# Kernel optimization log

Measured on AMD Instinct MI355X. Metric: run time of the kernel, lower is better.

Reference implementation:

```python
import jax, jax.numpy as jnp
import numpy as np

DIM = 64
HEADS = 4            # self.num_heads = 2 * num_heads(=2)
SMK = 5
KS = 7
EPS = 1e-5
SCALE = (DIM // HEADS) ** -0.5


def pool_mat(n, out=7):
    # AdaptiveAvgPool2d bin matrix: P[i, j] = 1/size if floor(i*n/out) <= j < ceil((i+1)*n/out)
    P = np.zeros((out, n), np.float32)
    for i in range(out):
        s = (i * n) // out
        e = -((-(i + 1) * n) // out)
        P[i, s:e] = 1.0 / (e - s)
    return jnp.asarray(P)


def bn(x, g, b, m, v):
    # inference BatchNorm2d on [B,C,H,W]
    return (x - m[:, None, None]) * (g[:, None, None] * jax.lax.rsqrt(v[:, None, None] + EPS)) + b[:, None, None]


def conv1x1(x, w):
    return jnp.einsum('oi,bihw->bohw', w, x)


def rpb_bias(rpb, H, W, k):
    # replicate apply_rpb gather indexing (incl. the flip over flattened HW)
    rs = 2 * k - 1
    ih0 = np.arange(k)
    idx_k = (ih0[:, None] * rs + ih0[None, :]).reshape(-1)        # [k*k]
    rh = np.ones(k, np.int64); rh[k // 2] = H - (k - 1)
    rw = np.ones(k, np.int64); rw[k // 2] = W - (k - 1)
    ih = np.repeat(ih0, rh)                                       # [H]
    iw = np.repeat(ih0, rw)                                       # [W]
    bias_hw = ih[:, None] * rs + iw[None, :]                      # [H,W]
    bias_idx = (bias_hw[..., None] + idx_k).reshape(-1, k * k)[::-1].copy()  # [H*W,k*k]
    flat = rpb.reshape(rpb.shape[0], -1)                          # [G, rs*rs]
    return flat[:, bias_idx].reshape(1, rpb.shape[0], H, W, k * k)


def na2d_av(attn, value, k):
    # NATTEN-style neighborhood AV: window start clamped to stay in-bounds
    B, G, H, W, _ = attn.shape
    si = np.clip(np.arange(H) - k // 2, 0, H - k)
    sj = np.clip(np.arange(W) - k // 2, 0, W - k)
    ii = si[:, None] + np.arange(k)    # [H,k]
    jj = sj[:, None] + np.arange(k)    # [W,k]
    v = value[:, :, ii][:, :, :, :, jj]         # [B,G,H,k,W,k,C]
    a = attn.reshape(B, G, H, W, k, k)
    return jnp.einsum('bghwij,bghiwjc->bghwc', a, v)


def reference(x, wq_w, wq_g, wq_b, wq_m, wq_v,
              wk_w, wk_g, wk_b, wk_m, wk_v,
              proj_w, proj_b, rpb1, rpb2,
              dy_w, dy_g, dy_b, dy_m, dy_v):
    B, C, H, W = x.shape
    G = HEADS
    q, kctx = jnp.split(x, 2, axis=1)                      # [B,C/2,H,W] each
    q = bn(conv1x1(q, wq_w), wq_g, wq_b, wq_m, wq_v) * SCALE
    Ph, Pw = pool_mat(H), pool_mat(W)
    kp = jnp.einsum('ph,bchw,qw->bcpq', Ph, kctx, Pw)      # adaptive avg pool to 7x7
    k = bn(conv1x1(kp, wk_w), wk_g, wk_b, wk_m, wk_v)
    q = q.reshape(B, G, -1, H * W)                          # b g c n
    k = k.reshape(B, G, -1, 49)                             # b g c l
    w = jnp.einsum('bgcn,bgcl->bgnl', q, k)
    w = w.transpose(0, 3, 1, 2)                             # b l g n
    w = jnp.einsum('ol,blgn->bogn', proj_w, w) + proj_b[None, :, None, None]  # b (74) g n
    w = w.transpose(0, 2, 3, 1).reshape(B, G, H, W, SMK * SMK + KS * KS)
    attn1 = w[..., :SMK * SMK]
    attn2 = w[..., SMK * SMK:]
    attn1 = jax.nn.softmax(attn1 + rpb_bias(rpb1, H, W, SMK), axis=-1)
    attn2 = jax.nn.softmax(attn2 + rpb_bias(rpb2, H, W, KS), axis=-1)
    c = C // (2 * G)
    value = x.reshape(B, 2, G, c, H, W).transpose(1, 0, 2, 4, 5, 3)  # m b g h w c
    x1 = na2d_av(attn1, value[0], SMK)
    x2 = na2d_av(attn2, value[1], KS)
    out = jnp.concatenate([x1, x2], axis=1)                 # b (2g) h w c
    out = out.transpose(0, 1, 4, 2, 3).reshape(B, C, H, W)  # b (g c) h w
    return bn(conv1x1(out, dy_w), dy_g, dy_b, dy_m, dy_v)


def setup_inputs() -> dict:
    key = jax.random.key(0)
    ks = jax.random.split(key, 20)
    h = DIM // 2
    def bnp(k):
        k1, k2, k3, k4 = jax.random.split(k, 4)
        return (jax.random.uniform(k1, (0,)),)  # unused
    inp = {
        'x': jax.random.normal(ks[0], (8, DIM, 64, 64), jnp.float32),
        'wq_w': jax.random.normal(ks[1], (h, h), jnp.float32) * (h ** -0.5),
        'wq_g': jax.random.uniform(ks[2], (h,), jnp.float32, 0.5, 1.5),
        'wq_b': jax.random.normal(ks[3], (h,), jnp.float32) * 0.1,
        'wq_m': jax.random.normal(ks[4], (h,), jnp.float32) * 0.1,
        'wq_v': jax.random.uniform(ks[5], (h,), jnp.float32, 0.5, 1.5),
        'wk_w': jax.random.normal(ks[6], (h, h), jnp.float32) * (h ** -0.5),
        'wk_g': jax.random.uniform(ks[7], (h,), jnp.float32, 0.5, 1.5),
        'wk_b': jax.random.normal(ks[8], (h,), jnp.float32) * 0.1,
        'wk_m': jax.random.normal(ks[9], (h,), jnp.float32) * 0.1,
        'wk_v': jax.random.uniform(ks[10], (h,), jnp.float32, 0.5, 1.5),
        'proj_w': jax.random.normal(ks[11], (SMK * SMK + KS * KS, 49), jnp.float32) * (49 ** -0.5),
        'proj_b': jax.random.normal(ks[12], (SMK * SMK + KS * KS,), jnp.float32) * 0.02,
        'rpb1': jax.random.normal(ks[13], (HEADS, 2 * SMK - 1, 2 * SMK - 1), jnp.float32) * 0.02,
        'rpb2': jax.random.normal(ks[14], (HEADS, 2 * KS - 1, 2 * KS - 1), jnp.float32) * 0.02,
        'dy_w': jax.random.normal(ks[15], (DIM, DIM), jnp.float32) * (DIM ** -0.5),
        'dy_g': jax.random.uniform(ks[16], (DIM,), jnp.float32, 0.5, 1.5),
        'dy_b': jax.random.normal(ks[17], (DIM,), jnp.float32) * 0.1,
        'dy_m': jax.random.normal(ks[18], (DIM,), jnp.float32) * 0.1,
        'dy_v': jax.random.uniform(ks[19], (DIM,), jnp.float32, 0.5, 1.5),
    }
    return inp
```

## Files before the change

### kernel.cpp

```cpp
#include <hip/hip_runtime.h>

#define EPSV 1e-5f

__global__ __launch_bounds__(256) void pool_k_kernel(
    const float* __restrict__ x,
    const float* __restrict__ wk_w, const float* __restrict__ wk_g,
    const float* __restrict__ wk_b, const float* __restrict__ wk_m,
    const float* __restrict__ wk_v, float* __restrict__ kbuf)
{
  const int b = blockIdx.x / 7;
  const int p = blockIdx.x % 7;
  const int tid = threadIdx.x;
  __shared__ float s_tmp[32 * 64];
  __shared__ float s_kp[32 * 7];

  const int sh = (p * 64) / 7, eh = ((p + 1) * 64 + 6) / 7;
  const float invH = 1.0f / (float)(eh - sh);
  for (int idx = tid; idx < 2048; idx += 256) {
    const int c = idx >> 6, ww = idx & 63;
    const float* xp = x + ((size_t)(b * 64 + 32 + c)) * 4096 + ww;
    float s = 0.f;
    for (int hh = sh; hh < eh; ++hh) s += xp[hh * 64];
    s_tmp[idx] = s * invH;
  }
  __syncthreads();
  if (tid < 224) {
    const int c = tid / 7, q = tid % 7;
    const int sw = (q * 64) / 7, ew = ((q + 1) * 64 + 6) / 7;
    float s = 0.f;
    for (int ww = sw; ww < ew; ++ww) s += s_tmp[c * 64 + ww];
    s_kp[c * 7 + q] = s / (float)(ew - sw);
  }
  __syncthreads();
  if (tid < 224) {
    const int o = tid / 7, q = tid % 7;
    float s = 0.f;
#pragma unroll
    for (int i = 0; i < 32; i++) s += wk_w[o * 32 + i] * s_kp[i * 7 + q];
    const float sc = wk_g[o] * rsqrtf(wk_v[o] + EPSV);
    kbuf[(size_t)b * 1568 + o * 49 + p * 7 + q] = (s - wk_m[o]) * sc + wk_b[o];
  }
}

__global__ __launch_bounds__(512, 4) void contmix_main(
    const float* __restrict__ x,
    const float* __restrict__ wq_w, const float* __restrict__ wq_g,
    const float* __restrict__ wq_b, const float* __restrict__ wq_m,
    const float* __restrict__ wq_v,
    const float* __restrict__ proj_w, const float* __restrict__ proj_b,
    const float* __restrict__ rpb1, const float* __restrict__ rpb2,
    const float* __restrict__ dy_w, const float* __restrict__ dy_g,
    const float* __restrict__ dy_b, const float* __restrict__ dy_m,
    const float* __restrict__ dy_v,
    const float* __restrict__ kbuf,
    float* __restrict__ out)
{
  __shared__ float s_rpb1[4 * 81];
  __shared__ float s_rpb2[4 * 169];
  __shared__ float s_val[64 * 64];

  const int bx = blockIdx.x;
  const int b = bx >> 6;
  const int h = bx & 63;
  const int tid = threadIdx.x;
  const int w = tid & 63;
  const int bru = __builtin_amdgcn_readfirstlane(tid >> 8);
  const int gu  = __builtin_amdgcn_readfirstlane((tid >> 6) & 3);

  for (int i = tid; i < 324; i += 512) s_rpb1[i] = rpb1[i];
  for (int i = tid; i < 676; i += 512) s_rpb2[i] = rpb2[i];
  __syncthreads();

  const float* xb = x + (size_t)b * 64 * 4096;

  float q8[8];
#pragma unroll
  for (int o = 0; o < 8; o++) q8[o] = 0.f;
  {
    const float* wqr = wq_w + gu * 8 * 32;
#pragma unroll
    for (int i = 0; i < 32; i++) {
      const float xv = xb[i * 4096 + h * 64 + w];
#pragma unroll
      for (int o = 0; o < 8; o++) q8[o] += wqr[o * 32 + i] * xv;
    }
#pragma unroll
    for (int o = 0; o < 8; o++) {
      const int oc = gu * 8 + o;
      const float s = wq_g[oc] * rsqrtf(wq_v[oc] + EPSV);
      q8[o] = (q8[o] * s + (wq_b[oc] - wq_m[oc] * s)) * 0.25f;
    }
  }

  float wv[49];
  {
    const float* kkb = kbuf + (size_t)b * 1568 + gu * 392;
#pragma unroll
    for (int l = 0; l < 49; l++) {
      float s = 0.f;
#pragma unroll
      for (int c = 0; c < 8; c++) s += q8[c] * kkb[c * 49 + l];
      wv[l] = s;
    }
  }

  const int ph = 63 - h, pw = 63 - w;

  if (bru == 0) {
    const int bih5 = ph - min(max(ph - 2, 0), 59);
    const int biw5 = pw - min(max(pw - 2, 0), 59);
    const int si5 = min(max(h - 2, 0), 59), sj5 = min(max(w - 2, 0), 59);
    float l1[25];
#pragma unroll
    for (int o = 0; o < 25; o++) {
      float s = proj_b[o];
#pragma unroll
      for (int l = 0; l < 49; l++) s += proj_w[o * 49 + l] * wv[l];
      l1[o] = s;
    }
    const float* rp1 = s_rpb1 + gu * 81 + bih5 * 9 + biw5;
#pragma unroll
    for (int ki = 0; ki < 5; ki++)
#pragma unroll
      for (int kj = 0; kj < 5; kj++) l1[ki * 5 + kj] += rp1[ki * 9 + kj];

    float mx = l1[0];
#pragma unroll
    for (int o = 1; o < 25; o++) mx = fmaxf(mx, l1[o]);
    float sum = 0.f;
#pragma unroll
    for (int o = 0; o < 25; o++) {
      const float e = __expf(l1[o] - mx);
      l1[o] = e;
      sum += e;
    }
    const float inv = 1.f / sum;

    float acc[8];
#pragma unroll
    for (int c = 0; c < 8; c++) acc[c] = 0.f;
    const float* vb = xb + gu * 8 * 4096;
#pragma unroll
    for (int i = 0; i < 5; i++) {
      const float* vr = vb + (si5 + i) * 64 + sj5;
#pragma unroll
      for (int j = 0; j < 5; j++) {
        const float a = l1[i * 5 + j];
#pragma unroll
        for (int c = 0; c < 8; c++) acc[c] += a * vr[c * 4096 + j];
      }
    }
#pragma unroll
    for (int c = 0; c < 8; c++) s_val[(gu * 8 + c) * 64 + w] = acc[c] * inv;
  } else {
    const int bih7 = ph - min(max(ph - 3, 0), 57);
    const int biw7 = pw - min(max(pw - 3, 0), 57);
    const int si7 = min(max(h - 3, 0), 57), sj7 = min(max(w - 3, 0), 57);
    float l2[49];
#pragma unroll
    for (int o = 0; o < 49; o++) {
      float s = proj_b[25 + o];
#pragma unroll
      for (int l = 0; l < 49; l++) s += proj_w[(25 + o) * 49 + l] * wv[l];
      l2[o] = s;
    }
    const float* rp2 = s_rpb2 + gu * 169 + bih7 * 13 + biw7;
#pragma unroll
    for (int ki = 0; ki < 7; ki++)
#pragma unroll
      for (int kj = 0; kj < 7; kj++) l2[ki * 7 + kj] += rp2[ki * 13 + kj];

    float mx = l2[0];
#pragma unroll
    for (int o = 1; o < 49; o++) mx = fmaxf(mx, l2[o]);
    float sum = 0.f;
#pragma unroll
    for (int o = 0; o < 49; o++) {
      const float e = __expf(l2[o] - mx);
      l2[o] = e;
      sum += e;
    }
    const float inv = 1.f / sum;

    float acc[8];
#pragma unroll
    for (int c = 0; c < 8; c++) acc[c] = 0.f;
    const float* vb = xb + (32 + gu * 8) * 4096;
#pragma unroll
    for (int i = 0; i < 7; i++) {
      const float* vr = vb + (si7 + i) * 64 + sj7;
#pragma unroll
      for (int j = 0; j < 7; j++) {
        const float a = l2[i * 7 + j];
#pragma unroll
        for (int c = 0; c < 8; c++) acc[c] += a * vr[c * 4096 + j];
      }
    }
#pragma unroll
    for (int c = 0; c < 8; c++) s_val[(32 + gu * 8 + c) * 64 + w] = acc[c] * inv;
  }

  __syncthreads();

  {
    const int ogu = __builtin_amdgcn_readfirstlane(tid >> 6);
    float facc[8];
#pragma unroll
    for (int oo = 0; oo < 8; oo++) facc[oo] = 0.f;
    const float* dwr = dy_w + ogu * 8 * 64;
#pragma unroll
    for (int i = 0; i < 64; i++) {
      const float v = s_val[i * 64 + w];
#pragma unroll
      for (int oo = 0; oo < 8; oo++) facc[oo] += dwr[oo * 64 + i] * v;
    }
#pragma unroll
    for (int oo = 0; oo < 8; oo++) {
      const int oc = ogu * 8 + oo;
      const float sc = dy_g[oc] * rsqrtf(dy_v[oc] + EPSV);
      out[((size_t)(b * 64 + oc)) * 4096 + h * 64 + w] =
          (facc[oo] - dy_m[oc]) * sc + dy_b[oc];
    }
  }
}

extern "C" void kernel_launch(void* const* d_in, const int* in_sizes, int n_in,
                              void* d_out, int out_size, void* d_ws, size_t ws_size,
                              hipStream_t stream)
{
  const float* x      = (const float*)d_in[0];
  const float* wq_w   = (const float*)d_in[1];
  const float* wq_g   = (const float*)d_in[2];
  const float* wq_b   = (const float*)d_in[3];
  const float* wq_m   = (const float*)d_in[4];
  const float* wq_v   = (const float*)d_in[5];
  const float* wk_w   = (const float*)d_in[6];
  const float* wk_g   = (const float*)d_in[7];
  const float* wk_b   = (const float*)d_in[8];
  const float* wk_m   = (const float*)d_in[9];
  const float* wk_v   = (const float*)d_in[10];
  const float* proj_w = (const float*)d_in[11];
  const float* proj_b = (const float*)d_in[12];
  const float* rpb1   = (const float*)d_in[13];
  const float* rpb2   = (const float*)d_in[14];
  const float* dy_w   = (const float*)d_in[15];
  const float* dy_g   = (const float*)d_in[16];
  const float* dy_b   = (const float*)d_in[17];
  const float* dy_m   = (const float*)d_in[18];
  const float* dy_v   = (const float*)d_in[19];

  float* kbuf = (float*)d_ws;

  pool_k_kernel<<<56, 256, 0, stream>>>(x, wk_w, wk_g, wk_b, wk_m, wk_v, kbuf);
  contmix_main<<<512, 512, 0, stream>>>(x, wq_w, wq_g, wq_b, wq_m, wq_v,
                                        proj_w, proj_b, rpb1, rpb2,
                                        dy_w, dy_g, dy_b, dy_m, dy_v,
                                        kbuf, (float*)d_out);
}
```

Baseline: 196.0 us.

## Pre-transpose weights and stream k-projection fused into logit accumulation

Adds a prep kernel that writes transposed, padded copies of wq, proj and dy weights to workspace, and stores the pooled key buffer transposed so each position's 8 channels are contiguous. The main kernel no longer keeps a 49-element wv array; it computes each wv[l] on the fly and scatters it into the logit accumulators, which cuts register pressure and lets weight loads be contiguous and vectorizable. The occupancy hint is relaxed from 4 to 2 blocks per unit. The cost is an extra kernel launch and a changed register/occupancy balance.

```diff
diff --git a/kernel.cpp b/kernel.cpp
--- a/kernel.cpp
+++ b/kernel.cpp
@@ -1,12 +1,44 @@
 #include <hip/hip_runtime.h>
 
 #define EPSV 1e-5f
+
+#define OFF_PW1T 12544
+#define OFF_PW2T 14112
+#define OFF_WQT  17248
+#define OFF_DYT  18272
+
+__global__ __launch_bounds__(512) void prep_weights(
+    const float* __restrict__ wq_w, const float* __restrict__ proj_w,
+    const float* __restrict__ dy_w, float* __restrict__ ws)
+{
+  const int t = blockIdx.x * 512 + threadIdx.x;
+  float* wqT  = ws + OFF_WQT;
+  float* pw1T = ws + OFF_PW1T;
+  float* pw2T = ws + OFF_PW2T;
+  float* dyT  = ws + OFF_DYT;
+  for (int idx = t; idx < 1024; idx += 8192) {
+    const int i = idx >> 5, o = idx & 31;
+    wqT[idx] = wq_w[o * 32 + i];
+  }
+  for (int idx = t; idx < 1568; idx += 8192) {
+    const int l = idx >> 5, o = idx & 31;
+    pw1T[idx] = (o < 25) ? proj_w[o * 49 + l] : 0.f;
+  }
+  for (int idx = t; idx < 3136; idx += 8192) {
+    const int l = idx >> 6, o = idx & 63;
+    pw2T[idx] = (o < 49) ? proj_w[(25 + o) * 49 + l] : 0.f;
+  }
+  for (int idx = t; idx < 4096; idx += 8192) {
+    const int i = idx >> 6, o = idx & 63;
+    dyT[idx] = dy_w[o * 64 + i];
+  }
+}
 
 __global__ __launch_bounds__(256) void pool_k_kernel(
     const float* __restrict__ x,
     const float* __restrict__ wk_w, const float* __restrict__ wk_g,
     const float* __restrict__ wk_b, const float* __restrict__ wk_m,
-    const float* __restrict__ wk_v, float* __restrict__ kbuf)
+    const float* __restrict__ wk_v, float* __restrict__ kbufT)
 {
   const int b = blockIdx.x / 7;
   const int p = blockIdx.x % 7;
@@ -38,21 +70,21 @@
 #pragma unroll
     for (int i = 0; i < 32; i++) s += wk_w[o * 32 + i] * s_kp[i * 7 + q];
     const float sc = wk_g[o] * rsqrtf(wk_v[o] + EPSV);
-    kbuf[(size_t)b * 1568 + o * 49 + p * 7 + q] = (s - wk_m[o]) * sc + wk_b[o];
-  }
-}
-
-__global__ __launch_bounds__(512, 4) void contmix_main(
+    const int g = o >> 3, c = o & 7, l = p * 7 + q;
+    kbufT[(((size_t)b * 4 + g) * 49 + l) * 8 + c] =
+        (s - wk_m[o]) * sc + wk_b[o];
+  }
+}
+
+__global__ __launch_bounds__(512, 2) void contmix_main(
     const float* __restrict__ x,
-    const float* __restrict__ wq_w, const float* __restrict__ wq_g,
-    const float* __restrict__ wq_b, const float* __restrict__ wq_m,
-    const float* __restrict__ wq_v,
-    const float* __restrict__ proj_w, const float* __restrict__ proj_b,
+    const float* __restrict__ wq_g, const float* __restrict__ wq_b,
+    const float* __restrict__ wq_m, const float* __restrict__ wq_v,
+    const float* __restrict__ proj_b,
     const float* __restrict__ rpb1, const float* __restrict__ rpb2,
-    const float* __restrict__ dy_w, const float* __restrict__ dy_g,
-    const float* __restrict__ dy_b, const float* __restrict__ dy_m,
-    const float* __restrict__ dy_v,
-    const float* __restrict__ kbuf,
+    const float* __restrict__ dy_g, const float* __restrict__ dy_b,
+    const float* __restrict__ dy_m, const float* __restrict__ dy_v,
+    const float* __restrict__ ws,
     float* __restrict__ out)
 {
   __shared__ float s_rpb1[4 * 81];
@@ -77,12 +109,12 @@
 #pragma unroll
   for (int o = 0; o < 8; o++) q8[o] = 0.f;
   {
-    const float* wqr = wq_w + gu * 8 * 32;
+    const float* wqt = ws + OFF_WQT + gu * 8;
 #pragma unroll
     for (int i = 0; i < 32; i++) {
       const float xv = xb[i * 4096 + h * 64 + w];
 #pragma unroll
-      for (int o = 0; o < 8; o++) q8[o] += wqr[o * 32 + i] * xv;
+      for (int o = 0; o < 8; o++) q8[o] += wqt[i * 32 + o] * xv;
     }
 #pragma unroll
     for (int o = 0; o < 8; o++) {
@@ -92,17 +124,7 @@
     }
   }
 
-  float wv[49];
-  {
-    const float* kkb = kbuf + (size_t)b * 1568 + gu * 392;
-#pragma unroll
-    for (int l = 0; l < 49; l++) {
-      float s = 0.f;
-#pragma unroll
-      for (int c = 0; c < 8; c++) s += q8[c] * kkb[c * 49 + l];
-      wv[l] = s;
-    }
-  }
+  const float* kt = ws + ((size_t)b * 4 + gu) * 392;
 
   const int ph = 63 - h, pw = 63 - w;
 
@@ -112,11 +134,16 @@
     const int si5 = min(max(h - 2, 0), 59), sj5 = min(max(w - 2, 0), 59);
     float l1[25];
 #pragma unroll
-    for (int o = 0; o < 25; o++) {
-      float s = proj_b[o];
-#pragma unroll
-      for (int l = 0; l < 49; l++) s += proj_w[o * 49 + l] * wv[l];
-      l1[o] = s;
+    for (int o = 0; o < 25; o++) l1[o] = proj_b[o];
+    const float* p1 = ws + OFF_PW1T;
+#pragma unroll 4
+    for (int l = 0; l < 49; l++) {
+      float a = 0.f;
+#pragma unroll
+      for (int c = 0; c < 8; c++) a += q8[c] * kt[l * 8 + c];
+      const float* pr = p1 + l * 32;
+#pragma unroll
+      for (int o = 0; o < 25; o++) l1[o] += pr[o] * a;
     }
     const float* rp1 = s_rpb1 + gu * 81 + bih5 * 9 + biw5;
 #pragma unroll
@@ -158,11 +185,16 @@
     const int si7 = min(max(h - 3, 0), 57), sj7 = min(max(w - 3, 0), 57);
     float l2[49];
 #pragma unroll
-    for (int o = 0; o < 49; o++) {
-      float s = proj_b[25 + o];
-#pragma unroll
-      for (int l = 0; l < 49; l++) s += proj_w[(25 + o) * 49 + l] * wv[l];
-      l2[o] = s;
+    for (int o = 0; o < 49; o++) l2[o] = proj_b[25 + o];
+    const float* p2 = ws + OFF_PW2T;
+#pragma unroll 4
+    for (int l = 0; l < 49; l++) {
+      float a = 0.f;
+#pragma unroll
+      for (int c = 0; c < 8; c++) a += q8[c] * kt[l * 8 + c];
+      const float* pr = p2 + l * 64;
+#pragma unroll
+      for (int o = 0; o < 49; o++) l2[o] += pr[o] * a;
     }
     const float* rp2 = s_rpb2 + gu * 169 + bih7 * 13 + biw7;
 #pragma unroll
@@ -207,12 +239,12 @@
     float facc[8];
 #pragma unroll
     for (int oo = 0; oo < 8; oo++) facc[oo] = 0.f;
-    const float* dwr = dy_w + ogu * 8 * 64;
+    const float* dyt = ws + OFF_DYT + ogu * 8;
 #pragma unroll
     for (int i = 0; i < 64; i++) {
       const float v = s_val[i * 64 + w];
 #pragma unroll
-      for (int oo = 0; oo < 8; oo++) facc[oo] += dwr[oo * 64 + i] * v;
+      for (int oo = 0; oo < 8; oo++) facc[oo] += dyt[i * 64 + oo] * v;
     }
 #pragma unroll
     for (int oo = 0; oo < 8; oo++) {
@@ -249,11 +281,12 @@
   const float* dy_m   = (const float*)d_in[18];
   const float* dy_v   = (const float*)d_in[19];
 
-  float* kbuf = (float*)d_ws;
-
-  pool_k_kernel<<<56, 256, 0, stream>>>(x, wk_w, wk_g, wk_b, wk_m, wk_v, kbuf);
-  contmix_main<<<512, 512, 0, stream>>>(x, wq_w, wq_g, wq_b, wq_m, wq_v,
-                                        proj_w, proj_b, rpb1, rpb2,
-                                        dy_w, dy_g, dy_b, dy_m, dy_v,
-                                        kbuf, (float*)d_out);
-}
+  float* ws = (float*)d_ws;
+
+  prep_weights<<<16, 512, 0, stream>>>(wq_w, proj_w, dy_w, ws);
+  pool_k_kernel<<<56, 256, 0, stream>>>(x, wk_w, wk_g, wk_b, wk_m, wk_v, ws);
+  contmix_main<<<512, 512, 0, stream>>>(x, wq_g, wq_b, wq_m, wq_v,
+                                        proj_b, rpb1, rpb2,
+                                        dy_g, dy_b, dy_m, dy_v,
+                                        ws, (float*)d_out);
+}
```

Measured after the change: 199.7 us. About the same (+1.9%).

## Fold proj_w into pooled keys, transpose weights, vectorize neighborhood loads

Applied to the files above, without the earlier changes.

Adds a per-batch-per-head kernel that precomputes proj_w·K (74x8) so the main kernel computes logits directly from the 8-dim query. This replaces the 49-wide intermediate and its 49x74 matvec per pixel. Also pre-transposes wq_w and dy_w into the workspace so per-thread weight reads become contiguous, and loads neighborhood value rows as 4-wide vectors. It adds two small extra launches and lowers the occupancy hint from 4 to 3 blocks.

```diff
diff --git a/kernel.cpp b/kernel.cpp
--- a/kernel.cpp
+++ b/kernel.cpp
@@ -1,6 +1,30 @@
 #include <hip/hip_runtime.h>
 
 #define EPSV 1e-5f
+
+#define OFF_W    12544
+#define OFF_WQT  31488
+#define OFF_DYT  32512
+
+typedef float f4u __attribute__((ext_vector_type(4), aligned(4)));
+
+__global__ __launch_bounds__(512) void prep_weights(
+    const float* __restrict__ wq_w, const float* __restrict__ dy_w,
+    float* __restrict__ ws)
+{
+  const int t = blockIdx.x * 512 + threadIdx.x;
+  float* wqT = ws + OFF_WQT;
+  float* dyT = ws + OFF_DYT;
+  if (t < 1024) {
+    const int i = t >> 5, o = t & 31;
+    wqT[t] = wq_w[o * 32 + i];
+  }
+  const int t2 = t - 1024;
+  if (t2 >= 0 && t2 < 4096) {
+    const int i = t2 >> 6, o = t2 & 63;
+    dyT[t2] = dy_w[o * 64 + i];
+  }
+}
 
 __global__ __launch_bounds__(256) void pool_k_kernel(
     const float* __restrict__ x,
@@ -38,21 +62,39 @@
 #pragma unroll
     for (int i = 0; i < 32; i++) s += wk_w[o * 32 + i] * s_kp[i * 7 + q];
     const float sc = wk_g[o] * rsqrtf(wk_v[o] + EPSV);
-    kbuf[(size_t)b * 1568 + o * 49 + p * 7 + q] = (s - wk_m[o]) * sc + wk_b[o];
-  }
-}
-
-__global__ __launch_bounds__(512, 4) void contmix_main(
+    const int g = o >> 3, c = o & 7, l = p * 7 + q;
+    kbuf[(((size_t)b * 4 + g) * 8 + c) * 49 + l] =
+        (s - wk_m[o]) * sc + wk_b[o];
+  }
+}
+
+__global__ __launch_bounds__(256) void fold_w_kernel(
+    const float* __restrict__ proj_w, const float* __restrict__ ws_in,
+    float* __restrict__ Wout)
+{
+  const int bg = blockIdx.x;
+  const int tid = threadIdx.x;
+  __shared__ float s_k[392];
+  for (int i = tid; i < 392; i += 256) s_k[i] = ws_in[(size_t)bg * 392 + i];
+  __syncthreads();
+  for (int idx = tid; idx < 592; idx += 256) {
+    const int o = idx >> 3, c = idx & 7;
+    float s = 0.f;
+#pragma unroll
+    for (int l = 0; l < 49; l++) s += proj_w[o * 49 + l] * s_k[c * 49 + l];
+    Wout[(size_t)bg * 592 + idx] = s;
+  }
+}
+
+__global__ __launch_bounds__(512, 3) void contmix_main(
     const float* __restrict__ x,
-    const float* __restrict__ wq_w, const float* __restrict__ wq_g,
-    const float* __restrict__ wq_b, const float* __restrict__ wq_m,
-    const float* __restrict__ wq_v,
-    const float* __restrict__ proj_w, const float* __restrict__ proj_b,
+    const float* __restrict__ wq_g, const float* __restrict__ wq_b,
+    const float* __restrict__ wq_m, const float* __restrict__ wq_v,
+    const float* __restrict__ proj_b,
     const float* __restrict__ rpb1, const float* __restrict__ rpb2,
-    const float* __restrict__ dy_w, const float* __restrict__ dy_g,
-    const float* __restrict__ dy_b, const float* __restrict__ dy_m,
-    const float* __restrict__ dy_v,
-    const float* __restrict__ kbuf,
+    const float* __restrict__ dy_g, const float* __restrict__ dy_b,
+    const float* __restrict__ dy_m, const float* __restrict__ dy_v,
+    const float* __restrict__ ws,
     float* __restrict__ out)
 {
   __shared__ float s_rpb1[4 * 81];
@@ -77,12 +119,12 @@
 #pragma unroll
   for (int o = 0; o < 8; o++) q8[o] = 0.f;
   {
-    const float* wqr = wq_w + gu * 8 * 32;
+    const float* wqt = ws + OFF_WQT + gu * 8;
 #pragma unroll
     for (int i = 0; i < 32; i++) {
       const float xv = xb[i * 4096 + h * 64 + w];
 #pragma unroll
-      for (int o = 0; o < 8; o++) q8[o] += wqr[o * 32 + i] * xv;
+      for (int o = 0; o < 8; o++) q8[o] += wqt[i * 32 + o] * xv;
     }
 #pragma unroll
     for (int o = 0; o < 8; o++) {
@@ -92,17 +134,7 @@
     }
   }
 
-  float wv[49];
-  {
-    const float* kkb = kbuf + (size_t)b * 1568 + gu * 392;
-#pragma unroll
-    for (int l = 0; l < 49; l++) {
-      float s = 0.f;
-#pragma unroll
-      for (int c = 0; c < 8; c++) s += q8[c] * kkb[c * 49 + l];
-      wv[l] = s;
-    }
-  }
+  const float* Wr = ws + OFF_W + (size_t)(b * 4 + gu) * 592;
 
   const int ph = 63 - h, pw = 63 - w;
 
@@ -113,9 +145,10 @@
     float l1[25];
 #pragma unroll
     for (int o = 0; o < 25; o++) {
+      const float* wo = Wr + o * 8;
       float s = proj_b[o];
 #pragma unroll
-      for (int l = 0; l < 49; l++) s += proj_w[o * 49 + l] * wv[l];
+      for (int c = 0; c < 8; c++) s += wo[c] * q8[c];
       l1[o] = s;
     }
     const float* rp1 = s_rpb1 + gu * 81 + bih5 * 9 + biw5;
@@ -142,12 +175,15 @@
     const float* vb = xb + gu * 8 * 4096;
 #pragma unroll
     for (int i = 0; i < 5; i++) {
-      const float* vr = vb + (si5 + i) * 64 + sj5;
-#pragma unroll
-      for (int j = 0; j < 5; j++) {
-        const float a = l1[i * 5 + j];
-#pragma unroll
-        for (int c = 0; c < 8; c++) acc[c] += a * vr[c * 4096 + j];
+      const float a0 = l1[i * 5 + 0], a1 = l1[i * 5 + 1], a2 = l1[i * 5 + 2];
+      const float a3 = l1[i * 5 + 3], a4 = l1[i * 5 + 4];
+      const float* vr0 = vb + (si5 + i) * 64 + sj5;
+#pragma unroll
+      for (int c = 0; c < 8; c++) {
+        const float* vr = vr0 + c * 4096;
+        const f4u f = *(const f4u*)vr;
+        const float v4 = vr[4];
+        acc[c] += a0 * f.x + a1 * f.y + a2 * f.z + a3 * f.w + a4 * v4;
       }
     }
 #pragma unroll
@@ -159,9 +195,10 @@
     float l2[49];
 #pragma unroll
     for (int o = 0; o < 49; o++) {
+      const float* wo = Wr + (25 + o) * 8;
       float s = proj_b[25 + o];
 #pragma unroll
-      for (int l = 0; l < 49; l++) s += proj_w[(25 + o) * 49 + l] * wv[l];
+      for (int c = 0; c < 8; c++) s += wo[c] * q8[c];
       l2[o] = s;
     }
     const float* rp2 = s_rpb2 + gu * 169 + bih7 * 13 + biw7;
@@ -188,12 +225,17 @@
     const float* vb = xb + (32 + gu * 8) * 4096;
 #pragma unroll
     for (int i = 0; i < 7; i++) {
-      const float* vr = vb + (si7 + i) * 64 + sj7;
-#pragma unroll
-      for (int j = 0; j < 7; j++) {
-        const float a = l2[i * 7 + j];
-#pragma unroll
-        for (int c = 0; c < 8; c++) acc[c] += a * vr[c * 4096 + j];
+      const float a0 = l2[i * 7 + 0], a1 = l2[i * 7 + 1], a2 = l2[i * 7 + 2];
+      const float a3 = l2[i * 7 + 3], a4 = l2[i * 7 + 4], a5 = l2[i * 7 + 5];
+      const float a6 = l2[i * 7 + 6];
+      const float* vr0 = vb + (si7 + i) * 64 + sj7;
+#pragma unroll
+      for (int c = 0; c < 8; c++) {
+        const float* vr = vr0 + c * 4096;
+        const f4u fa = *(const f4u*)vr;
+        const f4u fb = *(const f4u*)(vr + 3);
+        acc[c] += a0 * fa.x + a1 * fa.y + a2 * fa.z + a3 * fa.w +
+                  a4 * fb.y + a5 * fb.z + a6 * fb.w;
       }
     }
 #pragma unroll
@@ -207,12 +249,12 @@
     float facc[8];
 #pragma unroll
     for (int oo = 0; oo < 8; oo++) facc[oo] = 0.f;
-    const float* dwr = dy_w + ogu * 8 * 64;
+    const float* dyt = ws + OFF_DYT + ogu * 8;
 #pragma unroll
     for (int i = 0; i < 64; i++) {
       const float v = s_val[i * 64 + w];
 #pragma unroll
-      for (int oo = 0; oo < 8; oo++) facc[oo] += dwr[oo * 64 + i] * v;
+      for (int oo = 0; oo < 8; oo++) facc[oo] += dyt[i * 64 + oo] * v;
     }
 #pragma unroll
     for (int oo = 0; oo < 8; oo++) {
@@ -249,11 +291,13 @@
   const float* dy_m   = (const float*)d_in[18];
   const float* dy_v   = (const float*)d_in[19];
 
-  float* kbuf = (float*)d_ws;
-
-  pool_k_kernel<<<56, 256, 0, stream>>>(x, wk_w, wk_g, wk_b, wk_m, wk_v, kbuf);
-  contmix_main<<<512, 512, 0, stream>>>(x, wq_w, wq_g, wq_b, wq_m, wq_v,
-                                        proj_w, proj_b, rpb1, rpb2,
-                                        dy_w, dy_g, dy_b, dy_m, dy_v,
-                                        kbuf, (float*)d_out);
-}
+  float* ws = (float*)d_ws;
+
+  prep_weights<<<10, 512, 0, stream>>>(wq_w, dy_w, ws);
+  pool_k_kernel<<<56, 256, 0, stream>>>(x, wk_w, wk_g, wk_b, wk_m, wk_v, ws);
+  fold_w_kernel<<<32, 256, 0, stream>>>(proj_w, ws, ws + OFF_W);
+  contmix_main<<<512, 512, 0, stream>>>(x, wq_g, wq_b, wq_m, wq_v,
+                                        proj_b, rpb1, rpb2,
+                                        dy_g, dy_b, dy_m, dy_v,
+                                        ws, (float*)d_out);
+}
```

Result: faster. 165.9 us (-15.3%).
